# Performance work log

Hardware: AMD Instinct MI355X
Metric: run time of the kernel (lower is better)

Reference implementation:

```python
import jax, jax.numpy as jnp
import numpy as np

N = 62          # EEG channels (nodes per graph)
B = 512         # graphs in batch
K = 2           # SGConv propagation steps
F_IN = 128
H = 64
C = 3


def _complete_graph_edge_index():
    # edge e = g*N*N + i*N + j connects node g*N+i -> g*N+j,
    # matching edge_weight = Wsym.reshape(-1).repeat(B) ordering.
    base = np.arange(N)
    ii = np.tile(np.repeat(base, N), B)
    jj = np.tile(np.tile(base, N), B)
    off = np.repeat(np.arange(B) * N, N * N)
    return jnp.asarray(np.stack([off + ii, off + jj]).astype(np.int32))


def setup_inputs() -> dict:
    key = jax.random.key(0)
    ks = jax.random.split(key, 6)
    n_total = B * N
    x = jax.random.normal(ks[0], (n_total, F_IN), dtype=jnp.float32)
    edge_weight_tril = jax.random.normal(ks[1], (N * (N + 1) // 2,), dtype=jnp.float32)
    W1 = jax.random.normal(ks[2], (H, F_IN), dtype=jnp.float32) * (1.0 / np.sqrt(F_IN))
    b1 = jax.random.normal(ks[3], (H,), dtype=jnp.float32) * 0.01
    W2 = jax.random.normal(ks[4], (C, H), dtype=jnp.float32) * (1.0 / np.sqrt(H))
    b2 = jax.random.normal(ks[5], (C,), dtype=jnp.float32) * 0.01
    edge_index = _complete_graph_edge_index()
    batch = jnp.asarray(np.repeat(np.arange(B), N).astype(np.int32))
    return {"x": x, "edge_weight_tril": edge_weight_tril, "W1": W1, "b1": b1,
            "W2": W2, "b2": b2, "edge_index": edge_index, "batch": batch,
            "batch_size": B}


def reference(x, edge_weight_tril, W1, b1, W2, b2, edge_index, batch, batch_size):
    n_total = x.shape[0]
    # rebuild symmetric dense adjacency from lower-tri params
    xs, ys = np.tril_indices(N)
    Wm = jnp.zeros((N, N), dtype=x.dtype).at[xs, ys].set(edge_weight_tril)
    Wsym = Wm + Wm.T - jnp.diag(jnp.diag(Wm))
    ew = jnp.tile(Wsym.reshape(-1), batch_size)            # [B*N*N]

    row, col = edge_index[0], edge_index[1]
    # symmetric normalization (graph already contains self loops)
    deg = jax.ops.segment_sum(jnp.abs(ew), row, num_segments=n_total)
    dinv = jnp.where(deg > 0, deg ** -0.5, 0.0)
    norm = dinv[row] * ew * dinv[col]                      # [E]

    # K-step SGConv propagation: gather, scale, scatter-add
    h = x
    for _ in range(K):
        h = jax.ops.segment_sum(norm[:, None] * h[row], col, num_segments=n_total)

    h = jax.nn.relu(h @ W1.T + b1)                         # [n_total, H]
    pooled = jax.ops.segment_sum(h, batch, num_segments=batch_size)  # global_add_pool
    latent_v = pooled                                      # dropout in eval mode = identity
    logits = latent_v @ W2.T + b2
    logp = jax.nn.log_softmax(logits, axis=-1)
    return latent_v, logp
```

## Files before the change

### kernel.cpp

```cpp
#include <hip/hip_runtime.h>
#include <math.h>

#define NN  62
#define BGR 512
#define FIN 128
#define HD  64
#define NC  3

typedef __attribute__((ext_vector_type(8))) short          bf16x8;
typedef __attribute__((ext_vector_type(4))) float          f32x4;
typedef __attribute__((ext_vector_type(4))) unsigned short us4;

static __device__ __forceinline__ unsigned short f2bf(float f) {
    union { float f; unsigned u; } v; v.f = f;
    unsigned u = v.u;
    return (unsigned short)((u + 0x7fffu + ((u >> 16) & 1u)) >> 16);
}
static __device__ __forceinline__ float bf2f(unsigned short h) {
    union { unsigned u; float f; } v; v.u = ((unsigned)h) << 16;
    return v.f;
}


__global__ __launch_bounds__(256) void prep_kernel(const float* __restrict__ tril,
                                                   const float* __restrict__ W1,
                                                   unsigned short* __restrict__ wsu) {
    __shared__ float LDSF[1984 + 64 + 4096];
    const int t = threadIdx.x;
    const int b = blockIdx.x;

    if (b == 4) {
        for (int e = t; e < HD * FIN; e += 256) {
            int h = e >> 7, f = e & 127;
            float w = W1[e];
            unsigned short hi = f2bf(w);
            unsigned short lo = f2bf(w - bf2f(hi));
            wsu[9216  + h * 136 + f] = hi;
            wsu[17920 + h * 136 + f] = lo;
        }
        return;
    }

    float* trilS = LDSF;
    float* dinv  = LDSF + 1984;
    float* Ac    = LDSF + 2048;

    for (int e = t; e < NN * (NN + 1) / 2; e += 256) trilS[e] = tril[e];
    __syncthreads();
    if (t < NN) {
        float s = 0.f;
        for (int j = 0; j < NN; ++j) {
            int hi = max(t, j), lo = min(t, j);
            s += fabsf(trilS[hi * (hi + 1) / 2 + lo]);
        }
        dinv[t] = (s > 0.f) ? (1.0f / sqrtf(s)) : 0.f;
    }
    __syncthreads();
    for (int e = t; e < 64 * 64; e += 256) {
        int i = e >> 6, j = e & 63;
        float v = 0.f;
        if (i < NN && j < NN) {
            int hi = max(i, j), lo = min(i, j);
            v = dinv[i] * trilS[hi * (hi + 1) / 2 + lo] * dinv[j];
        }
        Ac[e] = v;
    }
    __syncthreads();
    {
        const int il = t >> 4, j4 = t & 15;
        const int i = 16 * b + il;
        const float4* Ac4 = (const float4*)Ac;
        float4 s4 = {0.f, 0.f, 0.f, 0.f};
        for (int k = 0; k < NN; ++k) {
            float a = Ac[i * 64 + k];
            float4 av = Ac4[k * 16 + j4];
            s4.x += a * av.x; s4.y += a * av.y; s4.z += a * av.z; s4.w += a * av.w;
        }
        us4 hh, ll;
        hh[0] = f2bf(s4.x); ll[0] = f2bf(s4.x - bf2f(hh[0]));
        hh[1] = f2bf(s4.y); ll[1] = f2bf(s4.y - bf2f(hh[1]));
        hh[2] = f2bf(s4.z); ll[2] = f2bf(s4.z - bf2f(hh[2]));
        hh[3] = f2bf(s4.w); ll[3] = f2bf(s4.w - bf2f(hh[3]));
        *(us4*)&wsu[       i * 72 + 4 * j4] = hh;
        *(us4*)&wsu[4608 + i * 72 + 4 * j4] = ll;
    }
}

__global__ __launch_bounds__(256) void gcn_fused(
    const float* __restrict__ x, const unsigned short* __restrict__ wsu,
    const float* __restrict__ b1, const float* __restrict__ W2,
    const float* __restrict__ b2, float* __restrict__ out) {
    __shared__ unsigned short SH[34816];
    __shared__ float TAIL[64 * 17 + 64 + 64];
    float* partial = TAIL;
    float* pooledS = TAIL + 1088;
    float* b1S     = TAIL + 1152;

    const int t = threadIdx.x;
    const int g = blockIdx.x;
    const int lane = t & 63, wv = t >> 6, quad = lane >> 4, l15 = lane & 15;

    if (t < 16) *(float4*)&b1S[4 * t] = ((const float4*)b1)[t];

    const float4* xg4 = (const float4*)(x + (size_t)g * NN * FIN);
    for (int e = t; e < 2048; e += 256) {
        int row = e >> 5, k4 = e & 31;
        float4 v = {0.f, 0.f, 0.f, 0.f};
        if (e < 1984) v = xg4[e];
        us4 hh, ll;
        hh[0] = f2bf(v.x); ll[0] = f2bf(v.x - bf2f(hh[0]));
        hh[1] = f2bf(v.y); ll[1] = f2bf(v.y - bf2f(hh[1]));
        hh[2] = f2bf(v.z); ll[2] = f2bf(v.z - bf2f(hh[2]));
        hh[3] = f2bf(v.w); ll[3] = f2bf(v.w - bf2f(hh[3]));
        *(us4*)&SH[       row * 136 + k4 * 4] = hh;
        *(us4*)&SH[8704 + row * 136 + k4 * 4] = ll;
    }
    {
        const float4* wsrc = (const float4*)(wsu + 9216);
        for (int e = t; e < 2176; e += 256) *(float4*)&SH[17408 + e * 8] = wsrc[e];
    }
    __syncthreads();

    f32x4 y0 = {0,0,0,0}, y1 = {0,0,0,0}, y2 = {0,0,0,0}, y3 = {0,0,0,0};
    {
        const int arow = (16 * wv + l15) * 136 + quad * 8;
#pragma unroll
        for (int c = 0; c < 4; ++c) {
            bf16x8 ahi = *(bf16x8*)&SH[arow + c * 32];
            bf16x8 alo = *(bf16x8*)&SH[8704 + arow + c * 32];
#define P1TILE(ACC, NT) { \
            int bo = (16 * NT + l15) * 136 + quad * 8 + c * 32; \
            bf16x8 bhi = *(bf16x8*)&SH[17408 + bo]; \
            bf16x8 blo = *(bf16x8*)&SH[26112 + bo]; \
            ACC = __builtin_amdgcn_mfma_f32_16x16x32_bf16(ahi, bhi, ACC, 0, 0, 0); \
            ACC = __builtin_amdgcn_mfma_f32_16x16x32_bf16(ahi, blo, ACC, 0, 0, 0); \
            ACC = __builtin_amdgcn_mfma_f32_16x16x32_bf16(alo, bhi, ACC, 0, 0, 0); \
            ACC = __builtin_amdgcn_mfma_f32_16x16x32_bf16(alo, blo, ACC, 0, 0, 0); }
            P1TILE(y0, 0) P1TILE(y1, 1) P1TILE(y2, 2) P1TILE(y3, 3)
#undef P1TILE
        }
    }
    __syncthreads();

    {
        const int mbase = 16 * wv + quad * 4;
#define YTW(ACC, NT) { \
        int n = 16 * NT + l15; \
        us4 hh, ll; \
        hh[0] = f2bf(ACC[0]); ll[0] = f2bf(ACC[0] - bf2f(hh[0])); \
        hh[1] = f2bf(ACC[1]); ll[1] = f2bf(ACC[1] - bf2f(hh[1])); \
        hh[2] = f2bf(ACC[2]); ll[2] = f2bf(ACC[2] - bf2f(hh[2])); \
        hh[3] = f2bf(ACC[3]); ll[3] = f2bf(ACC[3] - bf2f(hh[3])); \
        *(us4*)&SH[       n * 72 + mbase] = hh; \
        *(us4*)&SH[4608 + n * 72 + mbase] = ll; }
        YTW(y0, 0) YTW(y1, 1) YTW(y2, 2) YTW(y3, 3)
#undef YTW
    }
    {
        const float4* a2src = (const float4*)wsu;
        for (int e = t; e < 1152; e += 256) *(float4*)&SH[9216 + e * 8] = a2src[e];
    }
    __syncthreads();

    f32x4 z0 = {0,0,0,0}, z1 = {0,0,0,0}, z2 = {0,0,0,0}, z3 = {0,0,0,0};
    {
        const int arow = 9216 + (16 * wv + l15) * 72 + quad * 8;
#pragma unroll
        for (int c = 0; c < 2; ++c) {
            bf16x8 ahi = *(bf16x8*)&SH[arow + c * 32];
            bf16x8 alo = *(bf16x8*)&SH[4608 + arow + c * 32];
#define P2TILE(ACC, NT) { \
            int bo = (16 * NT + l15) * 72 + quad * 8 + c * 32; \
            bf16x8 bhi = *(bf16x8*)&SH[bo]; \
            bf16x8 blo = *(bf16x8*)&SH[4608 + bo]; \
            ACC = __builtin_amdgcn_mfma_f32_16x16x32_bf16(ahi, bhi, ACC, 0, 0, 0); \
            ACC = __builtin_amdgcn_mfma_f32_16x16x32_bf16(ahi, blo, ACC, 0, 0, 0); \
            ACC = __builtin_amdgcn_mfma_f32_16x16x32_bf16(alo, bhi, ACC, 0, 0, 0); \
            ACC = __builtin_amdgcn_mfma_f32_16x16x32_bf16(alo, blo, ACC, 0, 0, 0); }
            P2TILE(z0, 0) P2TILE(z1, 1) P2TILE(z2, 2) P2TILE(z3, 3)
#undef P2TILE
        }
    }

    {
        const int mbase = 16 * wv + quad * 4;
        const int slot = 4 * wv + quad;
#define POOL(ACC, NT) { \
        int n = 16 * NT + l15; \
        float bn = b1S[n]; \
        float p = 0.f; \
        if (mbase + 0 < 62) p += fmaxf(ACC[0] + bn, 0.f); \
        if (mbase + 1 < 62) p += fmaxf(ACC[1] + bn, 0.f); \
        if (mbase + 2 < 62) p += fmaxf(ACC[2] + bn, 0.f); \
        if (mbase + 3 < 62) p += fmaxf(ACC[3] + bn, 0.f); \
        partial[n * 17 + slot] = p; }
        POOL(z0, 0) POOL(z1, 1) POOL(z2, 2) POOL(z3, 3)
#undef POOL
    }
    __syncthreads();

    if (t < HD) {
        float s = 0.f;
        for (int q = 0; q < 16; ++q) s += partial[t * 17 + q];
        out[(size_t)g * HD + t] = s;
        pooledS[t] = s;
    }
    __syncthreads();

    if (t < NC) {
        float lg[NC];
#pragma unroll
        for (int c = 0; c < NC; ++c) {
            float zz = b2[c];
            for (int h = 0; h < HD; ++h) zz += pooledS[h] * W2[c * HD + h];
            lg[c] = zz;
        }
        float m = fmaxf(lg[0], fmaxf(lg[1], lg[2]));
        float lse = m + logf(expf(lg[0] - m) + expf(lg[1] - m) + expf(lg[2] - m));
        out[(size_t)BGR * HD + (size_t)g * NC + t] = lg[t] - lse;
    }
}

extern "C" void kernel_launch(void* const* d_in, const int* in_sizes, int n_in,
                              void* d_out, int out_size, void* d_ws, size_t ws_size,
                              hipStream_t stream) {
    const float* x    = (const float*)d_in[0];
    const float* tril = (const float*)d_in[1];
    const float* W1   = (const float*)d_in[2];
    const float* b1   = (const float*)d_in[3];
    const float* W2   = (const float*)d_in[4];
    const float* b2   = (const float*)d_in[5];
    float* out = (float*)d_out;
    unsigned short* wsu = (unsigned short*)d_ws;

    prep_kernel<<<5, 256, 0, stream>>>(tril, W1, wsu);
    gcn_fused<<<BGR, 256, 0, stream>>>(x, wsu, b1, W2, b2, out);
}
```

Baseline: 104.4 us.

## Fuse adjacency preparation into main kernel, dropping separate prep launch

Removes the prep kernel and has every block build the normalized adjacency, compute A² with MFMA, and split W1 into bf16 hi/lo itself. The main cost it targets is the extra kernel launch and the serialization between the two kernels. In exchange, all 512 blocks repeat the degree computation, the A² product and the W1 conversion, which adds per-block latency and extra barriers. It also replaces the serial log-softmax logit loop with a wavefront shuffle reduction.

```diff
diff --git a/kernel.cpp b/kernel.cpp
--- a/kernel.cpp
+++ b/kernel.cpp
@@ -21,80 +21,16 @@
     return v.f;
 }
 
-
-__global__ __launch_bounds__(256) void prep_kernel(const float* __restrict__ tril,
-                                                   const float* __restrict__ W1,
-                                                   unsigned short* __restrict__ wsu) {
-    __shared__ float LDSF[1984 + 64 + 4096];
-    const int t = threadIdx.x;
-    const int b = blockIdx.x;
-
-    if (b == 4) {
-        for (int e = t; e < HD * FIN; e += 256) {
-            int h = e >> 7, f = e & 127;
-            float w = W1[e];
-            unsigned short hi = f2bf(w);
-            unsigned short lo = f2bf(w - bf2f(hi));
-            wsu[9216  + h * 136 + f] = hi;
-            wsu[17920 + h * 136 + f] = lo;
-        }
-        return;
-    }
-
-    float* trilS = LDSF;
-    float* dinv  = LDSF + 1984;
-    float* Ac    = LDSF + 2048;
-
-    for (int e = t; e < NN * (NN + 1) / 2; e += 256) trilS[e] = tril[e];
-    __syncthreads();
-    if (t < NN) {
-        float s = 0.f;
-        for (int j = 0; j < NN; ++j) {
-            int hi = max(t, j), lo = min(t, j);
-            s += fabsf(trilS[hi * (hi + 1) / 2 + lo]);
-        }
-        dinv[t] = (s > 0.f) ? (1.0f / sqrtf(s)) : 0.f;
-    }
-    __syncthreads();
-    for (int e = t; e < 64 * 64; e += 256) {
-        int i = e >> 6, j = e & 63;
-        float v = 0.f;
-        if (i < NN && j < NN) {
-            int hi = max(i, j), lo = min(i, j);
-            v = dinv[i] * trilS[hi * (hi + 1) / 2 + lo] * dinv[j];
-        }
-        Ac[e] = v;
-    }
-    __syncthreads();
-    {
-        const int il = t >> 4, j4 = t & 15;
-        const int i = 16 * b + il;
-        const float4* Ac4 = (const float4*)Ac;
-        float4 s4 = {0.f, 0.f, 0.f, 0.f};
-        for (int k = 0; k < NN; ++k) {
-            float a = Ac[i * 64 + k];
-            float4 av = Ac4[k * 16 + j4];
-            s4.x += a * av.x; s4.y += a * av.y; s4.z += a * av.z; s4.w += a * av.w;
-        }
-        us4 hh, ll;
-        hh[0] = f2bf(s4.x); ll[0] = f2bf(s4.x - bf2f(hh[0]));
-        hh[1] = f2bf(s4.y); ll[1] = f2bf(s4.y - bf2f(hh[1]));
-        hh[2] = f2bf(s4.z); ll[2] = f2bf(s4.z - bf2f(hh[2]));
-        hh[3] = f2bf(s4.w); ll[3] = f2bf(s4.w - bf2f(hh[3]));
-        *(us4*)&wsu[       i * 72 + 4 * j4] = hh;
-        *(us4*)&wsu[4608 + i * 72 + 4 * j4] = ll;
-    }
-}
-
-__global__ __launch_bounds__(256) void gcn_fused(
-    const float* __restrict__ x, const unsigned short* __restrict__ wsu,
-    const float* __restrict__ b1, const float* __restrict__ W2,
-    const float* __restrict__ b2, float* __restrict__ out) {
+__global__ __launch_bounds__(256) void gcn_all(
+    const float* __restrict__ x, const float* __restrict__ tril,
+    const float* __restrict__ W1, const float* __restrict__ b1,
+    const float* __restrict__ W2, const float* __restrict__ b2,
+    float* __restrict__ out) {
     __shared__ unsigned short SH[34816];
-    __shared__ float TAIL[64 * 17 + 64 + 64];
+    __shared__ float TAIL[1088 + 64 + 64];
     float* partial = TAIL;
-    float* pooledS = TAIL + 1088;
-    float* b1S     = TAIL + 1152;
+    float* b1S     = TAIL + 1088;
+    float* dinvS   = TAIL + 1152;
 
     const int t = threadIdx.x;
     const int g = blockIdx.x;
@@ -115,9 +51,76 @@
         *(us4*)&SH[       row * 136 + k4 * 4] = hh;
         *(us4*)&SH[8704 + row * 136 + k4 * 4] = ll;
     }
-    {
-        const float4* wsrc = (const float4*)(wsu + 9216);
-        for (int e = t; e < 2176; e += 256) *(float4*)&SH[17408 + e * 8] = wsrc[e];
+    if (t < 64) {
+        float s = 0.f;
+        if (t < NN) {
+            for (int j = 0; j < NN; ++j) {
+                int hi = max(t, j), lo = min(t, j);
+                s += fabsf(tril[hi * (hi + 1) / 2 + lo]);
+            }
+            s = (s > 0.f) ? (1.0f / sqrtf(s)) : 0.f;
+        }
+        dinvS[t] = s;
+    }
+    __syncthreads();
+
+    for (int e4 = t; e4 < 1024; e4 += 256) {
+        int i = e4 >> 4, j0 = (e4 & 15) * 4;
+        float di = dinvS[i];
+        float4 dj4 = *(float4*)&dinvS[j0];
+        float dja[4] = {dj4.x, dj4.y, dj4.z, dj4.w};
+        us4 hh, ll;
+#pragma unroll
+        for (int r = 0; r < 4; ++r) {
+            int j = j0 + r;
+            float w = 0.f;
+            if (i < NN && j < NN) {
+                int hi = max(i, j), lo = min(i, j);
+                w = tril[hi * (hi + 1) / 2 + lo];
+            }
+            float v = di * w * dja[r];
+            hh[r] = f2bf(v);
+            ll[r] = f2bf(v - bf2f(hh[r]));
+        }
+        *(us4*)&SH[17408 + i * 72 + j0] = hh;
+        *(us4*)&SH[22016 + i * 72 + j0] = ll;
+    }
+    __syncthreads();
+
+    f32x4 za0 = {0,0,0,0}, za1 = {0,0,0,0}, za2 = {0,0,0,0}, za3 = {0,0,0,0};
+    {
+        const int arow = 17408 + (16 * wv + l15) * 72 + quad * 8;
+#pragma unroll
+        for (int c = 0; c < 2; ++c) {
+            bf16x8 ahi = *(bf16x8*)&SH[arow + c * 32];
+            bf16x8 alo = *(bf16x8*)&SH[4608 + arow + c * 32];
+#define ATILE(ACC, NT) { \
+            int bo = 17408 + (16 * NT + l15) * 72 + quad * 8 + c * 32; \
+            bf16x8 bhi = *(bf16x8*)&SH[bo]; \
+            bf16x8 blo = *(bf16x8*)&SH[4608 + bo]; \
+            ACC = __builtin_amdgcn_mfma_f32_16x16x32_bf16(ahi, bhi, ACC, 0, 0, 0); \
+            ACC = __builtin_amdgcn_mfma_f32_16x16x32_bf16(ahi, blo, ACC, 0, 0, 0); \
+            ACC = __builtin_amdgcn_mfma_f32_16x16x32_bf16(alo, bhi, ACC, 0, 0, 0); \
+            ACC = __builtin_amdgcn_mfma_f32_16x16x32_bf16(alo, blo, ACC, 0, 0, 0); }
+            ATILE(za0, 0) ATILE(za1, 1) ATILE(za2, 2) ATILE(za3, 3)
+#undef ATILE
+        }
+    }
+    __syncthreads();
+
+    {
+        const float4* w14 = (const float4*)W1;
+        for (int e = t; e < 2048; e += 256) {
+            int h = e >> 5, f4 = e & 31;
+            float4 v = w14[e];
+            us4 hh, ll;
+            hh[0] = f2bf(v.x); ll[0] = f2bf(v.x - bf2f(hh[0]));
+            hh[1] = f2bf(v.y); ll[1] = f2bf(v.y - bf2f(hh[1]));
+            hh[2] = f2bf(v.z); ll[2] = f2bf(v.z - bf2f(hh[2]));
+            hh[3] = f2bf(v.w); ll[3] = f2bf(v.w - bf2f(hh[3]));
+            *(us4*)&SH[17408 + h * 136 + f4 * 4] = hh;
+            *(us4*)&SH[26112 + h * 136 + f4 * 4] = ll;
+        }
     }
     __syncthreads();
 
@@ -144,21 +147,20 @@
 
     {
         const int mbase = 16 * wv + quad * 4;
-#define YTW(ACC, NT) { \
+#define SPLITW(ACC, NT, HIOFF, LOOFF) { \
         int n = 16 * NT + l15; \
         us4 hh, ll; \
         hh[0] = f2bf(ACC[0]); ll[0] = f2bf(ACC[0] - bf2f(hh[0])); \
         hh[1] = f2bf(ACC[1]); ll[1] = f2bf(ACC[1] - bf2f(hh[1])); \
         hh[2] = f2bf(ACC[2]); ll[2] = f2bf(ACC[2] - bf2f(hh[2])); \
         hh[3] = f2bf(ACC[3]); ll[3] = f2bf(ACC[3] - bf2f(hh[3])); \
-        *(us4*)&SH[       n * 72 + mbase] = hh; \
-        *(us4*)&SH[4608 + n * 72 + mbase] = ll; }
-        YTW(y0, 0) YTW(y1, 1) YTW(y2, 2) YTW(y3, 3)
-#undef YTW
-    }
-    {
-        const float4* a2src = (const float4*)wsu;
-        for (int e = t; e < 1152; e += 256) *(float4*)&SH[9216 + e * 8] = a2src[e];
+        *(us4*)&SH[(HIOFF) + n * 72 + mbase] = hh; \
+        *(us4*)&SH[(LOOFF) + n * 72 + mbase] = ll; }
+        SPLITW(y0, 0, 0, 4608) SPLITW(y1, 1, 0, 4608)
+        SPLITW(y2, 2, 0, 4608) SPLITW(y3, 3, 0, 4608)
+        SPLITW(za0, 0, 9216, 13824) SPLITW(za1, 1, 9216, 13824)
+        SPLITW(za2, 2, 9216, 13824) SPLITW(za3, 3, 9216, 13824)
+#undef SPLITW
     }
     __syncthreads();
 
@@ -201,23 +203,25 @@
 
     if (t < HD) {
         float s = 0.f;
+#pragma unroll
         for (int q = 0; q < 16; ++q) s += partial[t * 17 + q];
         out[(size_t)g * HD + t] = s;
-        pooledS[t] = s;
-    }
-    __syncthreads();
-
-    if (t < NC) {
-        float lg[NC];
-#pragma unroll
-        for (int c = 0; c < NC; ++c) {
-            float zz = b2[c];
-            for (int h = 0; h < HD; ++h) zz += pooledS[h] * W2[c * HD + h];
-            lg[c] = zz;
-        }
-        float m = fmaxf(lg[0], fmaxf(lg[1], lg[2]));
-        float lse = m + logf(expf(lg[0] - m) + expf(lg[1] - m) + expf(lg[2] - m));
-        out[(size_t)BGR * HD + (size_t)g * NC + t] = lg[t] - lse;
+        float l0 = s * W2[t];
+        float l1 = s * W2[64 + t];
+        float l2 = s * W2[128 + t];
+#pragma unroll
+        for (int off = 32; off > 0; off >>= 1) {
+            l0 += __shfl_down(l0, off);
+            l1 += __shfl_down(l1, off);
+            l2 += __shfl_down(l2, off);
+        }
+        if (t == 0) {
+            l0 += b2[0]; l1 += b2[1]; l2 += b2[2];
+            float m = fmaxf(l0, fmaxf(l1, l2));
+            float lse = m + logf(expf(l0 - m) + expf(l1 - m) + expf(l2 - m));
+            float* lp = out + (size_t)BGR * HD + (size_t)g * NC;
+            lp[0] = l0 - lse; lp[1] = l1 - lse; lp[2] = l2 - lse;
+        }
     }
 }
 
@@ -231,8 +235,6 @@
     const float* W2   = (const float*)d_in[4];
     const float* b2   = (const float*)d_in[5];
     float* out = (float*)d_out;
-    unsigned short* wsu = (unsigned short*)d_ws;
-
-    prep_kernel<<<5, 256, 0, stream>>>(tril, W1, wsu);
-    gcn_fused<<<BGR, 256, 0, stream>>>(x, wsu, b1, W2, b2, out);
-}
+
+    gcn_all<<<BGR, 256, 0, stream>>>(x, tril, W1, b1, W2, b2, out);
+}
```

Result: faster. 102.3 us (-2.1%).
